# Kernel tuning notes

Measured on AMD Instinct MI355X. Metric: run time of the kernel, lower is better.

The kernel has to match this reference:

```python
import jax, jax.numpy as jnp
import numpy as np

B, S, D, H = 4, 2048, 1024, 16
DEPTH = D // H
NEG = -1e9


def setup_inputs() -> dict:
    key = jax.random.key(0)
    ks = jax.random.split(key, 10)
    scale = 1.0 / np.sqrt(D)
    return {
        "query": jax.random.normal(ks[0], (B, S, D), jnp.float32),
        "key": jax.random.normal(ks[1], (B, S, D), jnp.float32),
        "value": jax.random.normal(ks[2], (B, S, D), jnp.float32),
        "mask": jnp.zeros((B, 1, 1, S), jnp.float32),
        "Wq": jax.random.normal(ks[3], (D, D), jnp.float32) * scale,
        "bq": jnp.zeros((D,), jnp.float32),
        "Wk": jax.random.normal(ks[4], (D, D), jnp.float32) * scale,
        "bk": jnp.zeros((D,), jnp.float32),
        "Wv": jax.random.normal(ks[5], (D, D), jnp.float32) * scale,
        "bv": jnp.zeros((D,), jnp.float32),
        "Wo": jax.random.normal(ks[6], (D, D), jnp.float32) * scale,
        "bo": jnp.zeros((D,), jnp.float32),
    }


def _split_heads(x):
    # [B, S, D] -> [B, H, S, depth]
    b, s, _ = x.shape
    return x.reshape(b, s, H, DEPTH).transpose(0, 2, 1, 3)


def reference(query, key, value, mask, Wq, bq, Wk, bk, Wv, bv, Wo, bo):
    q = _split_heads(query @ Wq + bq)
    k = _split_heads(key @ Wk + bk)
    v = _split_heads(value @ Wv + bv)
    # scaled dot-product attention
    logits = jnp.einsum("bhqd,bhkd->bhqk", q, k) / jnp.sqrt(
        jnp.asarray(DEPTH, jnp.float32))
    logits = logits + mask * NEG
    attn = jax.nn.softmax(logits, axis=-1)
    out = jnp.einsum("bhqk,bhkd->bhqd", attn, v)
    # merge heads: [B,H,S,depth] -> [B,S,D]
    out = out.transpose(0, 2, 1, 3).reshape(query.shape[0], -1, D)
    out = out @ Wo + bo
    return out, attn
```

## Files before the change

### kernel.cpp

```cpp
#include <hip/hip_runtime.h>
#include <stdint.h>


typedef float f32x4 __attribute__((ext_vector_type(4)));
typedef __bf16 bf16x8 __attribute__((ext_vector_type(8)));
typedef unsigned short u16x4 __attribute__((ext_vector_type(4)));
typedef unsigned short u16x8 __attribute__((ext_vector_type(8)));
typedef unsigned int u32x2 __attribute__((ext_vector_type(2)));

#define LOG2E 1.44269504088896340736f

static __device__ __forceinline__ f32x4 mfma16(bf16x8 a, bf16x8 b, f32x4 c) {
  return __builtin_amdgcn_mfma_f32_16x16x32_bf16(a, b, c, 0, 0, 0);
}
static __device__ __forceinline__ unsigned short bfc(float f) {
  return __builtin_bit_cast(unsigned short, (__bf16)f);
}
static __device__ __forceinline__ float e2(float x) { return __builtin_amdgcn_exp2f(x); }
static __device__ __forceinline__ float fb(unsigned int u) {
  return __builtin_bit_cast(float, u);
}

#define GLDS16(g, l)                                                    \
  __builtin_amdgcn_global_load_lds(                                     \
      (const __attribute__((address_space(1))) void*)(g),               \
      (__attribute__((address_space(3))) void*)(l), 16, 0, 0)

struct Ptr3 { const float* s[3]; unsigned short* d[3]; };
struct Ptr4 { const float* s[4]; unsigned short* d[4]; };
struct QKArgs {
  const unsigned short* A[2];
  const unsigned short* Bt[2];
  const float* bias[2];
  unsigned short* C[2];
};

__global__ void cvt3(Ptr3 p) {
  const int z = blockIdx.z;
  const int i = (blockIdx.x * 256 + threadIdx.x) * 4;
  f32x4 v = *(const f32x4*)(const void*)(p.s[z] + i);
  u16x4 o;
  o[0] = bfc(v[0]); o[1] = bfc(v[1]); o[2] = bfc(v[2]); o[3] = bfc(v[3]);
  *(u16x4*)(void*)(p.d[z] + i) = o;
}

__global__ void wtrans4(Ptr4 p) {
  __shared__ float t[32][33];
  const int z = blockIdx.z;
  const float* W = p.s[z];
  unsigned short* Wt = p.d[z];
  const int tx = threadIdx.x & 31, ty = threadIdx.x >> 5;
  const int n0 = blockIdx.x * 32, k0 = blockIdx.y * 32;
#pragma unroll
  for (int i = 0; i < 4; ++i)
    t[ty + i * 8][tx] = W[(size_t)(k0 + ty + i * 8) * 1024 + n0 + tx];
  __syncthreads();
#pragma unroll
  for (int i = 0; i < 4; ++i)
    Wt[(size_t)(n0 + ty + i * 8) * 1024 + k0 + tx] = bfc(t[tx][ty + i * 8]);
}

#define GEMM_PROLOG(Aptr, Btptr)                                        \
  __shared__ unsigned short sA[128 * 32];                               \
  __shared__ unsigned short sB[128 * 32];                               \
  const int tid = threadIdx.x;                                          \
  const int m0 = blockIdx.x << 7, n0 = blockIdx.y << 7;                 \
  const int w = tid >> 6, lane = tid & 63, g = lane >> 4, r = lane & 15;\
  const int wr = w >> 1, wc = w & 1;                                    \
  const int srow = tid >> 2;                                            \
  const int scol = (tid & 3) << 3;                                      \
  const unsigned short* ga = (Aptr) + (size_t)(m0 + srow) * 1024 + scol;\
  const unsigned short* gb = (Btptr) + (size_t)(n0 + srow) * 1024 + scol;\
  unsigned short* la = sA + tid * 8;                                    \
  unsigned short* lb = sB + tid * 8;

#define GEMM_KLOOP(SWAP)                                                \
  for (int kt = 0; kt < 32; ++kt) {                                     \
    const int ko = kt << 5;                                             \
    GLDS16(ga + ko, la);                                                \
    GLDS16(ga + ko + 64 * 1024, la + 64 * 32);                          \
    GLDS16(gb + ko, lb);                                                \
    GLDS16(gb + ko + 64 * 1024, lb + 64 * 32);                          \
    __syncthreads();                                                    \
    bf16x8 af[4], bfv[4];                                               \
    _Pragma("unroll")                                                   \
    for (int i = 0; i < 4; ++i) {                                       \
      af[i]  = *(const bf16x8*)(const void*)&sA[(wr * 64 + i * 16 + r) * 32 + g * 8]; \
      bfv[i] = *(const bf16x8*)(const void*)&sB[(wc * 64 + i * 16 + r) * 32 + g * 8]; \
    }                                                                   \
    _Pragma("unroll")                                                   \
    for (int i = 0; i < 4; ++i)                                         \
      _Pragma("unroll")                                                 \
      for (int j = 0; j < 4; ++j)                                       \
        acc[i][j] = (SWAP) ? mfma16(bfv[j], af[i], acc[i][j])           \
                           : mfma16(af[i], bfv[j], acc[i][j]);          \
    __syncthreads();                                                    \
  }

__global__ __launch_bounds__(256, 2) void gemm_qk(QKArgs args) {
  const int z = blockIdx.z;
  const f32x4 fz = {0.f, 0.f, 0.f, 0.f};
  f32x4 acc[4][4];
#pragma unroll
  for (int i = 0; i < 4; ++i)
#pragma unroll
    for (int j = 0; j < 4; ++j) acc[i][j] = fz;
  GEMM_PROLOG(args.A[z], args.Bt[z])
  GEMM_KLOOP(1)
  const float osc = (z == 0) ? (0.125f * LOG2E) : 1.0f;
  unsigned short* Cq = args.C[z];
  const float* bias = args.bias[z];
#pragma unroll
  for (int j = 0; j < 4; ++j) {
    const int nb = n0 + wc * 64 + j * 16 + g * 4;
    const f32x4 b4 = *(const f32x4*)(const void*)(bias + nb);
#pragma unroll
    for (int i = 0; i < 4; ++i) {
      const int m = m0 + wr * 64 + i * 16 + r;
      const int bb = m >> 11, s = m & 2047, hh = nb >> 6, d = nb & 63;
      u16x4 pk;
#pragma unroll
      for (int t = 0; t < 4; ++t) pk[t] = bfc((acc[i][j][t] + b4[t]) * osc);
      *(u16x4*)(void*)(Cq + (size_t)(bb * 16 + hh) * 131072 + (size_t)s * 64 + d) = pk;
    }
  }
}

__global__ __launch_bounds__(256, 2) void gemm_v(const unsigned short* __restrict__ A,
                                                 const unsigned short* __restrict__ Bt,
                                                 const float* __restrict__ bias,
                                                 unsigned short* __restrict__ C) {
  const f32x4 fz = {0.f, 0.f, 0.f, 0.f};
  f32x4 acc[4][4];
#pragma unroll
  for (int i = 0; i < 4; ++i)
#pragma unroll
    for (int j = 0; j < 4; ++j) acc[i][j] = fz;
  GEMM_PROLOG(A, Bt)
  GEMM_KLOOP(0)
#pragma unroll
  for (int j = 0; j < 4; ++j) {
    const int n = n0 + wc * 64 + j * 16 + r;
    const float bv = bias[n];
    const int hh = n >> 6, d = n & 63;
#pragma unroll
    for (int i = 0; i < 4; ++i) {
      const int m = m0 + wr * 64 + i * 16 + g * 4;
      const int bb = m >> 11, s = m & 2047;
      u16x4 pk;
#pragma unroll
      for (int t = 0; t < 4; ++t) pk[t] = bfc(acc[i][j][t] + bv);
      *(u16x4*)(void*)(C + (size_t)(bb * 16 + hh) * 131072 + (size_t)d * 2048 + s) = pk;
    }
  }
}

__global__ __launch_bounds__(256, 2) void gemm_o(const unsigned short* __restrict__ A,
                                                 const unsigned short* __restrict__ Bt,
                                                 const float* __restrict__ bias,
                                                 float* __restrict__ C) {
  const f32x4 fz = {0.f, 0.f, 0.f, 0.f};
  f32x4 acc[4][4];
#pragma unroll
  for (int i = 0; i < 4; ++i)
#pragma unroll
    for (int j = 0; j < 4; ++j) acc[i][j] = fz;
  GEMM_PROLOG(A, Bt)
  GEMM_KLOOP(1)
#pragma unroll
  for (int j = 0; j < 4; ++j) {
    const int nb = n0 + wc * 64 + j * 16 + g * 4;
    const f32x4 b4 = *(const f32x4*)(const void*)(bias + nb);
#pragma unroll
    for (int i = 0; i < 4; ++i) {
      const int m = m0 + wr * 64 + i * 16 + r;
      f32x4 c;
#pragma unroll
      for (int t = 0; t < 4; ++t) c[t] = acc[i][j][t] + b4[t];
      *(f32x4*)(void*)(C + (size_t)m * 1024 + nb) = c;
    }
  }
}

__global__ __launch_bounds__(256, 2) void attn_fused(const unsigned short* __restrict__ Qh,
                                                     const unsigned short* __restrict__ Kh,
                                                     const unsigned short* __restrict__ Vt,
                                                     const float* __restrict__ mask,
                                                     float* __restrict__ attn_out,
                                                     unsigned short* __restrict__ Obuf) {
  constexpr int PITCH = 138;
  __shared__ __align__(16) unsigned short PldsAll[4][64 * PITCH];
  __shared__ float sml[4][64];

  const int blk = (blockIdx.x & 7) * 256 + (blockIdx.x >> 3);
  const int bh = blk >> 5;
  const int q0 = (blk & 31) << 6;
  const int b = bh >> 4, h = bh & 15;
  const int tid = threadIdx.x;
  const int w = tid >> 6, lane = tid & 63, g = lane >> 4, r = lane & 15;
  const float NEGM = -1e9f * LOG2E;

  const unsigned short* Qb = Qh + (size_t)bh * (2048 * 64);
  const unsigned short* Kb = Kh + (size_t)bh * (2048 * 64);
  const unsigned short* Vb = Vt + (size_t)bh * (64 * 2048);
  const float* mb = mask + (size_t)b * 2048;
  const f32x4 fz = {0.f, 0.f, 0.f, 0.f};

  bf16x8 qf[4][2];
#pragma unroll
  for (int qc = 0; qc < 4; ++qc)
#pragma unroll
    for (int hf = 0; hf < 2; ++hf)
      qf[qc][hf] = *(const bf16x8*)(const void*)(Qb + (size_t)(q0 + qc * 16 + r) * 64 + hf * 32 + g * 8);

  float lreg[4] = {0.f, 0.f, 0.f, 0.f};

  for (int step = 0; step < 16; ++step) {
    const int kk = (w << 9) + (step << 5);
    bf16x8 kf[2][2];
#pragma unroll
    for (int ks = 0; ks < 2; ++ks)
#pragma unroll
      for (int hf = 0; hf < 2; ++hf)
        kf[ks][hf] = *(const bf16x8*)(const void*)(Kb + (size_t)(kk + ks * 16 + r) * 64 + hf * 32 + g * 8);
    f32x4 mv0 = *(const f32x4*)(const void*)(mb + kk + g * 4);
    f32x4 mv1 = *(const f32x4*)(const void*)(mb + kk + 16 + g * 4);
    f32x4 mp0, mp1;
#pragma unroll
    for (int j = 0; j < 4; ++j) { mp0[j] = mv0[j] * NEGM; mp1[j] = mv1[j] * NEGM; }

#pragma unroll
    for (int qc = 0; qc < 4; ++qc) {
      f32x4 s0 = fz, s1 = fz;
      s0 = mfma16(kf[0][0], qf[qc][0], s0);
      s0 = mfma16(kf[0][1], qf[qc][1], s0);
      s1 = mfma16(kf[1][0], qf[qc][0], s1);
      s1 = mfma16(kf[1][1], qf[qc][1], s1);
      float p = 0.f;
#pragma unroll
      for (int j = 0; j < 4; ++j) p += e2(s0[j] + mp0[j]) + e2(s1[j] + mp1[j]);
      lreg[qc] += p;
    }
  }
#pragma unroll
  for (int qc = 0; qc < 4; ++qc) {
    lreg[qc] += __shfl_xor(lreg[qc], 16);
    lreg[qc] += __shfl_xor(lreg[qc], 32);
  }
  if (lane < 16) {
#pragma unroll
    for (int qc = 0; qc < 4; ++qc) sml[w][qc * 16 + lane] = lreg[qc];
  }
  __syncthreads();
  float cL[4];
#pragma unroll
  for (int qc = 0; qc < 4; ++qc) {
    const int q = qc * 16 + r;
    cL[qc] = -__log2f(sml[0][q] + sml[1][q] + sml[2][q] + sml[3][q]);
  }

  f32x4 oacc[4][4];
#pragma unroll
  for (int i = 0; i < 4; ++i)
#pragma unroll
    for (int j = 0; j < 4; ++j) oacc[i][j] = fz;

  float* ab = attn_out + (size_t)bh * 2048 * 2048;
  unsigned short* Pw = &PldsAll[w][0];
  const int half = lane >> 5;
  const int l5 = lane & 31;

  for (int batch = 0; batch < 4; ++batch) {
#pragma unroll
    for (int sub = 0; sub < 4; ++sub) {
      const int step = batch * 4 + sub;
      const int kk = (w << 9) + (step << 5);
      bf16x8 kf[2][2];
#pragma unroll
      for (int ks = 0; ks < 2; ++ks)
#pragma unroll
        for (int hf = 0; hf < 2; ++hf)
          kf[ks][hf] = *(const bf16x8*)(const void*)(Kb + (size_t)(kk + ks * 16 + r) * 64 + hf * 32 + g * 8);
      f32x4 mv0 = *(const f32x4*)(const void*)(mb + kk + g * 4);
      f32x4 mv1 = *(const f32x4*)(const void*)(mb + kk + 16 + g * 4);
      f32x4 mp[2];
#pragma unroll
      for (int j = 0; j < 4; ++j) { mp[0][j] = mv0[j] * NEGM; mp[1][j] = mv1[j] * NEGM; }

#pragma unroll
      for (int ks = 0; ks < 2; ++ks) {
#pragma unroll
        for (int qc = 0; qc < 4; ++qc) {
          f32x4 s = fz;
          s = mfma16(kf[ks][0], qf[qc][0], s);
          s = mfma16(kf[ks][1], qf[qc][1], s);
          u16x4 pb;
#pragma unroll
          for (int j = 0; j < 4; ++j) pb[j] = bfc(e2(s[j] + mp[ks][j] + cL[qc]));
          *(u16x4*)(void*)(&Pw[(qc * 16 + r) * PITCH + sub * 32 + ks * 16 + g * 4]) = pb;
        }
      }
      bf16x8 vf[4];
#pragma unroll
      for (int dn = 0; dn < 4; ++dn)
        vf[dn] = *(const bf16x8*)(const void*)(Vb + (size_t)(dn * 16 + r) * 2048 + kk + g * 8);
#pragma unroll
      for (int qs = 0; qs < 4; ++qs) {
        const bf16x8 pa = *(const bf16x8*)(const void*)(&Pw[(qs * 16 + r) * PITCH + sub * 32 + g * 8]);
#pragma unroll
        for (int dn = 0; dn < 4; ++dn) oacc[qs][dn] = mfma16(pa, vf[dn], oacc[qs][dn]);
      }
    }
    const int colb = (w << 9) + (batch << 7);
#pragma unroll 4
    for (int i = 0; i < 32; ++i) {
      const int row = i * 2 + half;
      const u32x2 u = *(const u32x2*)(const void*)(&Pw[row * PITCH + l5 * 4]);
      f32x4 o;
      o[0] = fb(u[0] << 16);
      o[1] = fb(u[0] & 0xFFFF0000u);
      o[2] = fb(u[1] << 16);
      o[3] = fb(u[1] & 0xFFFF0000u);
      __builtin_nontemporal_store(
          o, (f32x4*)(void*)(ab + (size_t)(q0 + row) * 2048 + colb + l5 * 4));
    }
  }

  float (*Osum)[68] = reinterpret_cast<float (*)[68]>(&PldsAll[0][0]);
  for (int wv = 0; wv < 4; ++wv) {
    if (w == wv) {
#pragma unroll
      for (int qs = 0; qs < 4; ++qs)
#pragma unroll
        for (int dn = 0; dn < 4; ++dn)
#pragma unroll
          for (int j = 0; j < 4; ++j) {
            const int q = qs * 16 + g * 4 + j, d = dn * 16 + r;
            if (wv == 0) Osum[q][d] = oacc[qs][dn][j];
            else         Osum[q][d] += oacc[qs][dn][j];
          }
    }
    __syncthreads();
  }
  const int orow = tid >> 2, oc0 = (tid & 3) << 4;
#pragma unroll
  for (int hf2 = 0; hf2 < 2; ++hf2) {
    u16x8 pk;
#pragma unroll
    for (int j = 0; j < 8; ++j) pk[j] = bfc(Osum[orow][oc0 + hf2 * 8 + j]);
    *(u16x8*)(void*)(Obuf + (size_t)(b * 2048 + q0 + orow) * 1024 + h * 64 + oc0 + hf2 * 8) = pk;
  }
}

extern "C" void kernel_launch(void* const* d_in, const int* in_sizes, int n_in,
                              void* d_out, int out_size, void* d_ws, size_t ws_size,
                              hipStream_t stream) {
  const float* query = (const float*)d_in[0];
  const float* key_  = (const float*)d_in[1];
  const float* value = (const float*)d_in[2];
  const float* mask  = (const float*)d_in[3];
  const float* Wq = (const float*)d_in[4];
  const float* bq = (const float*)d_in[5];
  const float* Wk = (const float*)d_in[6];
  const float* bk = (const float*)d_in[7];
  const float* Wv = (const float*)d_in[8];
  const float* bv = (const float*)d_in[9];
  const float* Wo = (const float*)d_in[10];
  const float* bo = (const float*)d_in[11];

  uint8_t* ws = (uint8_t*)d_ws;
  unsigned short* XQ  = (unsigned short*)(ws);
  unsigned short* XK  = (unsigned short*)(ws + 16777216);
  unsigned short* XV  = (unsigned short*)(ws + 33554432);
  unsigned short* WTQ = (unsigned short*)(ws + 50331648);
  unsigned short* WTK = (unsigned short*)(ws + 52428800);
  unsigned short* WTV = (unsigned short*)(ws + 54525952);
  unsigned short* WTO = (unsigned short*)(ws + 56623104);
  unsigned short* QH  = (unsigned short*)(ws + 58720256);
  unsigned short* KH  = (unsigned short*)(ws + 75497472);
  unsigned short* VT  = (unsigned short*)(ws + 92274688);
  unsigned short* OB  = XQ;

  float* outp = (float*)d_out;
  float* attnp = outp + 8388608;

  Ptr3 pc = {{query, key_, value}, {XQ, XK, XV}};
  cvt3<<<dim3(8192, 1, 3), 256, 0, stream>>>(pc);
  Ptr4 pw = {{Wq, Wk, Wv, Wo}, {WTQ, WTK, WTV, WTO}};
  wtrans4<<<dim3(32, 32, 4), 256, 0, stream>>>(pw);
  QKArgs qk = {{XQ, XK}, {WTQ, WTK}, {bq, bk}, {QH, KH}};
  gemm_qk<<<dim3(64, 8, 2), 256, 0, stream>>>(qk);
  gemm_v<<<dim3(64, 8), 256, 0, stream>>>(XV, WTV, bv, VT);
  attn_fused<<<2048, 256, 0, stream>>>(QH, KH, VT, mask, attnp, OB);
  gemm_o<<<dim3(64, 8), 256, 0, stream>>>(OB, WTO, bo, outp);
}
```

Baseline: 449.3 us.

## Interleave key ranges across waves so attn writeback covers contiguous 512-column rows

Each wave now handles an interleaved 128-key slice inside each 512-key batch, so after a batch the four waves' P tiles together form a contiguous 512-column block. All waves sync and cooperatively write full 2 KB row segments of the attention matrix, using 16-byte LDS reads and two 16-byte nontemporal stores per lane. This makes the dominant global attn write more contiguous per row. The cost is two block-wide barriers per batch, which reduce independence between waves, plus extra LDS padding per slab.

```diff
diff --git a/kernel.cpp b/kernel.cpp
--- a/kernel.cpp
+++ b/kernel.cpp
@@ -6,7 +6,6 @@
 typedef __bf16 bf16x8 __attribute__((ext_vector_type(8)));
 typedef unsigned short u16x4 __attribute__((ext_vector_type(4)));
 typedef unsigned short u16x8 __attribute__((ext_vector_type(8)));
-typedef unsigned int u32x2 __attribute__((ext_vector_type(2)));
 
 #define LOG2E 1.44269504088896340736f
 
@@ -189,7 +188,8 @@
                                                      float* __restrict__ attn_out,
                                                      unsigned short* __restrict__ Obuf) {
   constexpr int PITCH = 138;
-  __shared__ __align__(16) unsigned short PldsAll[4][64 * PITCH];
+  constexpr int SLAB = 64 * PITCH + 16;
+  __shared__ __align__(16) unsigned short PldsAll[4][SLAB];
   __shared__ float sml[4][64];
 
   const int blk = (blockIdx.x & 7) * 256 + (blockIdx.x >> 3);
@@ -267,14 +267,11 @@
 
   float* ab = attn_out + (size_t)bh * 2048 * 2048;
   unsigned short* Pw = &PldsAll[w][0];
-  const int half = lane >> 5;
-  const int l5 = lane & 31;
 
   for (int batch = 0; batch < 4; ++batch) {
 #pragma unroll
     for (int sub = 0; sub < 4; ++sub) {
-      const int step = batch * 4 + sub;
-      const int kk = (w << 9) + (step << 5);
+      const int kk = (batch << 9) + (w << 7) + (sub << 5);
       bf16x8 kf[2][2];
 #pragma unroll
       for (int ks = 0; ks < 2; ++ks)
@@ -311,19 +308,26 @@
         for (int dn = 0; dn < 4; ++dn) oacc[qs][dn] = mfma16(pa, vf[dn], oacc[qs][dn]);
       }
     }
-    const int colb = (w << 9) + (batch << 7);
+    __syncthreads();
+    {
+      const unsigned short* Ps = &PldsAll[lane >> 4][0];
+      const int c16 = (lane & 15) << 3;
+      float* abb = ab + ((size_t)batch << 9);
 #pragma unroll 4
-    for (int i = 0; i < 32; ++i) {
-      const int row = i * 2 + half;
-      const u32x2 u = *(const u32x2*)(const void*)(&Pw[row * PITCH + l5 * 4]);
-      f32x4 o;
-      o[0] = fb(u[0] << 16);
-      o[1] = fb(u[0] & 0xFFFF0000u);
-      o[2] = fb(u[1] << 16);
-      o[3] = fb(u[1] & 0xFFFF0000u);
-      __builtin_nontemporal_store(
-          o, (f32x4*)(void*)(ab + (size_t)(q0 + row) * 2048 + colb + l5 * 4));
-    }
+      for (int i = 0; i < 16; ++i) {
+        const int row = (i << 2) + w;
+        const u16x8 uv = *(const u16x8*)(const void*)(&Ps[row * PITCH + c16]);
+        f32x4 o0, o1;
+        o0[0] = fb((unsigned)uv[0] << 16); o0[1] = fb((unsigned)uv[1] << 16);
+        o0[2] = fb((unsigned)uv[2] << 16); o0[3] = fb((unsigned)uv[3] << 16);
+        o1[0] = fb((unsigned)uv[4] << 16); o1[1] = fb((unsigned)uv[5] << 16);
+        o1[2] = fb((unsigned)uv[6] << 16); o1[3] = fb((unsigned)uv[7] << 16);
+        float* dst = abb + (size_t)(q0 + row) * 2048 + lane * 8;
+        __builtin_nontemporal_store(o0, (f32x4*)(void*)dst);
+        __builtin_nontemporal_store(o1, (f32x4*)(void*)(dst + 4));
+      }
+    }
+    __syncthreads();
   }
 
   float (*Osum)[68] = reinterpret_cast<float (*)[68]>(&PldsAll[0][0]);
```

Result: slower. 504.2 us (+12.2%).
